# Performance work log

Hardware: AMD Instinct MI355X
Metric: run time of the kernel (lower is better)

The kernel has to match this reference:

```python
import jax, jax.numpy as jnp
import numpy as np

B, S, D = 2, 4096, 512   # batch, seq_len, hidden_dim
H, E = 8, 64             # n_heads, head_dim


def setup_inputs() -> dict:
    key = jax.random.key(0)
    ks = jax.random.split(key, 14)
    s = 0.02  # init scale
    return {
        "x":  jax.random.normal(ks[0], (B, S, D), dtype=jnp.float32),
        # stacked per-head projection weights, stored as [H, in, out]
        "wq": jax.random.normal(ks[1], (H, D, E), dtype=jnp.float32) * s,
        "bq": jax.random.normal(ks[2], (H, E), dtype=jnp.float32) * s,
        "wk": jax.random.normal(ks[3], (H, D, E), dtype=jnp.float32) * s,
        "bk": jax.random.normal(ks[4], (H, E), dtype=jnp.float32) * s,
        "wv": jax.random.normal(ks[5], (H, D, E), dtype=jnp.float32) * s,
        "bv": jax.random.normal(ks[6], (H, E), dtype=jnp.float32) * s,
        "wo": jax.random.normal(ks[7], (H, E, D), dtype=jnp.float32) * s,
        "bo": jax.random.normal(ks[8], (H, D), dtype=jnp.float32) * s,
        # MLP: Linear(D,D) -> ReLU -> Linear(D,D), stored as [in, out]
        "w1": jax.random.normal(ks[9], (D, D), dtype=jnp.float32) * s,
        "b1": jax.random.normal(ks[10], (D,), dtype=jnp.float32) * s,
        "w2": jax.random.normal(ks[11], (D, D), dtype=jnp.float32) * s,
        "b2": jax.random.normal(ks[12], (D,), dtype=jnp.float32) * s,
    }


def reference(x, wq, bq, wk, bk, wv, bv, wo, bo, w1, b1, w2, b2):
    # Per-head projections, batched over heads: [B, H, S, E]
    q = jnp.einsum('bsd,hde->bhse', x, wq) + bq[None, :, None, :]
    k = jnp.einsum('bsd,hde->bhse', x, wk) + bk[None, :, None, :]
    v = jnp.einsum('bsd,hde->bhse', x, wv) + bv[None, :, None, :]
    scale = 1.0 / jnp.sqrt(jnp.asarray(q.shape[-1], q.dtype))
    scores = jnp.einsum('bhse,bhte->bhst', q, k) * scale  # [B,H,S,S]
    A = jax.nn.softmax(scores, axis=-1)
    ctx = jnp.einsum('bhst,bhte->bhse', A, v)             # [B,H,S,E]
    # w_o per head then sum over heads (each head adds its bias once)
    y = jnp.einsum('bhse,hed->bsd', ctx, wo) + jnp.sum(bo, axis=0)
    # MLP
    h = jax.nn.relu(y @ w1 + b1)
    return h @ w2 + b2
```

## Files before the change

### kernel.cpp

```cpp
#include <hip/hip_runtime.h>
#include <math.h>

#define Bsz 2
#define Sq  4096
#define Dm  512
#define Hn  8
#define Eh  64

typedef unsigned short u16;
typedef __attribute__((ext_vector_type(8))) short bf16x8;
typedef __attribute__((ext_vector_type(4))) float f32x4;
typedef __attribute__((ext_vector_type(16))) float f32x16;
typedef __attribute__((ext_vector_type(4))) unsigned short u16x4;

#define KSCALE 0.18033688011112042f

__device__ __forceinline__ u16 f2bf(float f) {
    unsigned int u = __float_as_uint(f);
    u += 0x7FFFu + ((u >> 16) & 1u);
    return (u16)(u >> 16);
}

__device__ __forceinline__ float fast_exp2(float x) {
#if defined(__HIP_DEVICE_COMPILE__) && __has_builtin(__builtin_amdgcn_exp2f)
    return __builtin_amdgcn_exp2f(x);
#else
    return exp2f(x);
#endif
}

__device__ __forceinline__ f32x16 mfma_32x32x16(bf16x8 a, bf16x8 b, f32x16 c) {
#if defined(__HIP_DEVICE_COMPILE__)
    return __builtin_amdgcn_mfma_f32_32x32x16_bf16(a, b, c, 0, 0, 0);
#else
    (void)a; (void)b;
    return c;
#endif
}

__device__ __forceinline__ unsigned cvt_pk_bf16(float lo, float hi) {
#if defined(__HIP_DEVICE_COMPILE__)
    unsigned r;
    asm("v_cvt_pk_bf16_f32 %0, %1, %2" : "=v"(r) : "v"(lo), "v"(hi));
    return r;
#else
    return ((unsigned)f2bf(hi) << 16) | (unsigned)f2bf(lo);
#endif
}

__device__ __forceinline__ void plane32_swap(unsigned &a, unsigned &b) {
#if defined(__HIP_DEVICE_COMPILE__)
    asm volatile("v_permlane32_swap_b32 %0, %1" : "+v"(a), "+v"(b));
#endif
}

__device__ __forceinline__ bf16x8 frag_of(unsigned a, unsigned b, unsigned c, unsigned d) {
    union { unsigned u[4]; bf16x8 v; } r;
    r.u[0] = a; r.u[1] = b; r.u[2] = c; r.u[3] = d;
    return r.v;
}

__device__ __forceinline__ void async16(const u16* g, u16* l) {
    __builtin_amdgcn_global_load_lds(
        (const __attribute__((address_space(1))) void*)g,
        (__attribute__((address_space(3))) void*)l, 16, 0, 0);
}

template<int TN, int NT>
__device__ __forceinline__ void gemm_core(
    const u16* __restrict__ A, const u16* __restrict__ WT,
    int m0, int n0, u16* Ast, u16* Bst, f32x4 (&acc)[4][NT])
{
    const int tid  = threadIdx.x;
    const int lane = tid & 63, wid = tid >> 6;
    const int l15  = lane & 15, quad = lane >> 4;
    const int wm = wid >> 1, wn = wid & 1;

    for (int kt = 0; kt < Dm / 64; ++kt) {
        const int k0 = kt * 64;
        __syncthreads();
#pragma unroll
        for (int j = 0; j < 4; ++j) {
            int ci = wid * 256 + j * 64 + lane;
            int row = ci >> 3, c = (ci & 7) ^ (row & 7);
            async16(&A[(size_t)(m0 + row) * Dm + k0 + c * 8],
                    &Ast[(size_t)(wid * 256 + j * 64) * 8]);
        }
#pragma unroll
        for (int j = 0; j < TN / 32; ++j) {
            int ci = wid * (TN * 2) + j * 64 + lane;
            int row = ci >> 3, c = (ci & 7) ^ (row & 7);
            async16(&WT[(size_t)(n0 + row) * Dm + k0 + c * 8],
                    &Bst[(size_t)(wid * (TN * 2) + j * 64) * 8]);
        }
        __syncthreads();
#pragma unroll
        for (int ks = 0; ks < 2; ++ks) {
            bf16x8 af[4], bfr[NT];
#pragma unroll
            for (int mt = 0; mt < 4; ++mt) {
                int r = wm * 64 + mt * 16 + l15;
                af[mt] = *(const bf16x8*)&Ast[(r * 8 + ((ks * 4 + quad) ^ (r & 7))) * 8];
            }
#pragma unroll
            for (int nt = 0; nt < NT; ++nt) {
                int n = wn * (TN / 2) + nt * 16 + l15;
                bfr[nt] = *(const bf16x8*)&Bst[(n * 8 + ((ks * 4 + quad) ^ (n & 7))) * 8];
            }
#pragma unroll
            for (int mt = 0; mt < 4; ++mt)
#pragma unroll
                for (int nt = 0; nt < NT; ++nt)
                    acc[mt][nt] = __builtin_amdgcn_mfma_f32_16x16x32_bf16(
                        af[mt], bfr[nt], acc[mt][nt], 0, 0, 0);
        }
    }
}

__global__ __launch_bounds__(256) void prep_kernel(
    const float* __restrict__ x,
    const float* __restrict__ wq, const float* __restrict__ wk,
    const float* __restrict__ wv, const float* __restrict__ wo,
    const float* __restrict__ w1, const float* __restrict__ w2,
    const float* __restrict__ bo,
    u16* __restrict__ xb, u16* __restrict__ wqkvT, u16* __restrict__ woT,
    u16* __restrict__ w1T, u16* __restrict__ w2T, float* __restrict__ bo_s)
{
    const int seg = blockIdx.y, bx = blockIdx.x, tid = threadIdx.x;
    if (seg == 0) {
        const float4* xi = (const float4*)x;
        for (int i = bx * 256 + tid; i < (Bsz * Sq * Dm) / 4; i += 64 * 256) {
            float4 v = xi[i];
            u16x4 o = {f2bf(v.x), f2bf(v.y), f2bf(v.z), f2bf(v.w)};
            *(u16x4*)&xb[(size_t)i * 4] = o;
        }
        return;
    }
    if (seg == 7) {
        int d = bx * 256 + tid;
        if (d < Dm) {
            float s = 0.0f;
#pragma unroll
            for (int h = 0; h < Hn; ++h) s += bo[h * Dm + d];
            bo_s[d] = s;
        }
        return;
    }
    __shared__ float t[64][65];
    const float* src; u16* dst; int ld_in;
    if (seg <= 3) {
        const float* w = (seg == 1) ? wq : (seg == 2) ? wk : wv;
        int head = bx >> 3, kt = bx & 7;
        src = w + (size_t)head * Dm * Eh + (size_t)kt * 64 * 64;
        ld_in = 64;
        dst = wqkvT + ((size_t)((seg - 1) * 8 + head) * 64) * 512 + kt * 64;
    } else {
        const float* w = (seg == 4) ? wo : (seg == 5) ? w1 : w2;
        u16* dT = (seg == 4) ? woT : (seg == 5) ? w1T : w2T;
        int tr = bx >> 3, tc = bx & 7;
        src = w + (size_t)(tr * 64) * 512 + tc * 64;
        ld_in = 512;
        dst = dT + (size_t)(tc * 64) * 512 + tr * 64;
    }
#pragma unroll
    for (int it = 0; it < 16; ++it) {
        int idx = it * 256 + tid;
        int r = idx >> 6, c = idx & 63;
        t[r][c] = src[(size_t)r * ld_in + c];
    }
    __syncthreads();
#pragma unroll
    for (int it = 0; it < 4; ++it) {
        int idx = it * 256 + tid;
        int oc = idx >> 4, og = idx & 15;
        u16x4 o;
#pragma unroll
        for (int j = 0; j < 4; ++j) o[j] = f2bf(t[og * 4 + j][oc]);
        *(u16x4*)&dst[(size_t)oc * 512 + og * 4] = o;
    }
}

__global__ __launch_bounds__(256, 2) void qkv_gemm(
    const u16* __restrict__ xb, const u16* __restrict__ wqkvT,
    const float* __restrict__ bq, const float* __restrict__ bk,
    const float* __restrict__ bv,
    u16* __restrict__ qb, u16* __restrict__ kb, u16* __restrict__ vbT)
{
    __shared__ __align__(16) u16 Ast[128 * 64];
    __shared__ __align__(16) u16 Bst[64 * 64];
    const int proj = blockIdx.y >> 3, h = blockIdx.y & 7;
    const u16* WT = wqkvT + (size_t)blockIdx.y * 64 * 512;

    f32x4 acc[4][2];
#pragma unroll
    for (int i = 0; i < 4; ++i)
#pragma unroll
        for (int j = 0; j < 2; ++j) acc[i][j] = (f32x4)0.0f;

    gemm_core<64, 2>(xb, WT, blockIdx.x * 128, 0, Ast, Bst, acc);

    const int tid = threadIdx.x;
    const int lane = tid & 63, wid = tid >> 6;
    const int l15 = lane & 15, quad = lane >> 4;
    const int wm = wid >> 1, wn = wid & 1;
    const float* bias = (proj == 0) ? bq : (proj == 1) ? bk : bv;

    const int mbase = blockIdx.x * 128 + wm * 64;
    const int b = mbase >> 12;
    const int sbase = (mbase & (Sq - 1));
    const int bh = b * Hn + h;

#pragma unroll
    for (int mt = 0; mt < 4; ++mt)
#pragma unroll
        for (int nt = 0; nt < 2; ++nt) {
            int e = wn * 32 + nt * 16 + l15;
            float bval = bias[h * Eh + e];
            int s = sbase + mt * 16 + quad * 4;
            if (proj == 2) {
                u16x4 o;
#pragma unroll
                for (int r = 0; r < 4; ++r) o[r] = f2bf(acc[mt][nt][r] + bval);
                *(u16x4*)&vbT[((size_t)bh * Eh + e) * Sq + s] = o;
            } else if (proj == 1) {
                for (int r = 0; r < 4; ++r)
                    kb[((size_t)bh * Sq + s + r) * Eh + e] =
                        f2bf((acc[mt][nt][r] + bval) * KSCALE);
            } else {
                for (int r = 0; r < 4; ++r)
                    qb[((size_t)bh * Sq + s + r) * Eh + e] = f2bf(acc[mt][nt][r] + bval);
            }
        }
}

__global__ __launch_bounds__(256, 2) void attn_kernel(
    const u16* __restrict__ qb, const u16* __restrict__ kb,
    const u16* __restrict__ vbT, u16* __restrict__ ctxb)
{
    __shared__ __align__(16) u16 kst[2][128 * 64];
    __shared__ __align__(16) u16 vst[2][64 * 128];

    const int tid  = threadIdx.x;
    const int lane = tid & 63, wid = tid >> 6;
    const int l31  = lane & 31, hh = lane >> 5;
    const int bh = blockIdx.y;
    const int q0 = blockIdx.x * 128;
    const int b = bh >> 3, h = bh & 7;

    const u16* qg = qb + (size_t)bh * Sq * Eh;
    const u16* kg = kb + (size_t)bh * Sq * Eh;
    const u16* vg = vbT + (size_t)bh * Eh * Sq;

    int krow[4], kcol[4], vrow[4], vcol[4];
#pragma unroll
    for (int j = 0; j < 4; ++j) {
        int ci = wid * 256 + j * 64 + lane;
        krow[j] = ci >> 3;
        kcol[j] = (ci & 7) ^ (krow[j] & 7);
        vrow[j] = ci >> 4;
        int vc  = ci & 15;
        vcol[j] = (vc & 8) | ((vc & 7) ^ (vrow[j] & 7));
    }

    bf16x8 qf[4];
    {
        const u16* qrow = &qg[(size_t)(q0 + wid * 32 + l31) * Eh + hh * 8];
#pragma unroll
        for (int ks = 0; ks < 4; ++ks)
            qf[ks] = *(const bf16x8*)&qrow[ks * 16];
    }

    f32x16 O[2];
    O[0] = (f32x16)0.0f;
    O[1] = (f32x16)0.0f;
    float lp = 0.0f;

#pragma unroll
    for (int j = 0; j < 4; ++j) {
        async16(&kg[(size_t)krow[j] * Eh + kcol[j] * 8],
                &kst[0][(wid * 256 + j * 64) * 8]);
        async16(&vg[(size_t)vrow[j] * Sq + vcol[j] * 8],
                &vst[0][(wid * 256 + j * 64) * 8]);
    }

    const int t7 = l31 & 7;

    for (int kt = 0; kt < Sq / 128; ++kt) {
        const int cur = kt & 1;
        __syncthreads();

        if (kt < Sq / 128 - 1) {
            const int t1 = (kt + 1) * 128;
#pragma unroll
            for (int j = 0; j < 4; ++j) {
                async16(&kg[(size_t)(t1 + krow[j]) * Eh + kcol[j] * 8],
                        &kst[cur ^ 1][(wid * 256 + j * 64) * 8]);
                async16(&vg[(size_t)vrow[j] * Sq + t1 + vcol[j] * 8],
                        &vst[cur ^ 1][(wid * 256 + j * 64) * 8]);
            }
        }

        const u16* kcur = kst[cur];
        const u16* vcur = vst[cur];

#pragma unroll
        for (int tt = 0; tt < 4; ++tt) {
            f32x16 S = (f32x16)0.0f;
            const int trow = (tt * 32 + l31) * 64;
#pragma unroll
            for (int ks = 0; ks < 4; ++ks) {
                bf16x8 kf = *(const bf16x8*)&kcur[trow + ((ks * 2 + hh) ^ t7) * 8];
                S = mfma_32x32x16(kf, qf[ks], S);
            }

            unsigned px[8];
#pragma unroll
            for (int j = 0; j < 8; ++j) {
                float p0 = fast_exp2(S[2 * j]);
                float p1 = fast_exp2(S[2 * j + 1]);
                lp += p0 + p1;
                px[j] = cvt_pk_bf16(p0, p1);
            }
            plane32_swap(px[0], px[2]);
            plane32_swap(px[1], px[3]);
            plane32_swap(px[4], px[6]);
            plane32_swap(px[5], px[7]);
            bf16x8 f0 = frag_of(px[0], px[1], px[2], px[3]);
            bf16x8 f1 = frag_of(px[4], px[5], px[6], px[7]);

#pragma unroll
            for (int et = 0; et < 2; ++et) {
                const int erow = (et * 32 + l31) * 128;
                int c0 = tt * 4 + hh;
                int c1 = c0 + 2;
                int g0 = (c0 & 8) | ((c0 & 7) ^ t7);
                int g1 = (c1 & 8) | ((c1 & 7) ^ t7);
                bf16x8 v0 = *(const bf16x8*)&vcur[erow + g0 * 8];
                bf16x8 v1 = *(const bf16x8*)&vcur[erow + g1 * 8];
                O[et] = mfma_32x32x16(v0, f0, O[et]);
                O[et] = mfma_32x32x16(v1, f1, O[et]);
            }
        }
    }

    lp += __shfl_xor(lp, 32, 64);
    const float rl = 1.0f / lp;

    const int qglob = q0 + wid * 32 + l31;
    u16* crow = ctxb + ((size_t)(b * Sq + qglob) * Hn + h) * Eh;
#pragma unroll
    for (int et = 0; et < 2; ++et)
#pragma unroll
        for (int g = 0; g < 4; ++g) {
            u16x4 o;
#pragma unroll
            for (int i = 0; i < 4; ++i) o[i] = f2bf(O[et][g * 4 + i] * rl);
            *(u16x4*)&crow[et * 32 + g * 8 + hh * 4] = o;
        }
}

template<int MODE>
__global__ __launch_bounds__(256, 2) void gemmMN(
    const u16* __restrict__ A, const u16* __restrict__ WT,
    const float* __restrict__ bias, void* __restrict__ Cout)
{
    __shared__ __align__(16) u16 Ast[128 * 64];
    __shared__ __align__(16) u16 Bst[64 * 64];

    f32x4 acc[4][2];
#pragma unroll
    for (int i = 0; i < 4; ++i)
#pragma unroll
        for (int j = 0; j < 2; ++j) acc[i][j] = (f32x4)0.0f;

    gemm_core<64, 2>(A, WT, blockIdx.x * 128, blockIdx.y * 64, Ast, Bst, acc);

    const int tid = threadIdx.x;
    const int lane = tid & 63, wid = tid >> 6;
    const int l15 = lane & 15, quad = lane >> 4;
    const int m0 = blockIdx.x * 128 + (wid >> 1) * 64;
    const int n0 = blockIdx.y * 64 + (wid & 1) * 32;

#pragma unroll
    for (int mt = 0; mt < 4; ++mt)
#pragma unroll
        for (int nt = 0; nt < 2; ++nt) {
            int col = n0 + nt * 16 + l15;
            float bval = bias[col];
#pragma unroll
            for (int r = 0; r < 4; ++r) {
                int row = m0 + mt * 16 + quad * 4 + r;
                float v = acc[mt][nt][r] + bval;
                if (MODE == 1) v = fmaxf(v, 0.0f);
                if (MODE == 2) ((float*)Cout)[(size_t)row * Dm + col] = v;
                else           ((u16*)Cout)[(size_t)row * Dm + col] = f2bf(v);
            }
        }
}

extern "C" void kernel_launch(void* const* d_in, const int* in_sizes, int n_in,
                              void* d_out, int out_size, void* d_ws, size_t ws_size,
                              hipStream_t stream)
{
    const float* x  = (const float*)d_in[0];
    const float* wq = (const float*)d_in[1];
    const float* bq = (const float*)d_in[2];
    const float* wk = (const float*)d_in[3];
    const float* bk = (const float*)d_in[4];
    const float* wv = (const float*)d_in[5];
    const float* bv = (const float*)d_in[6];
    const float* wo = (const float*)d_in[7];
    const float* bo = (const float*)d_in[8];
    const float* w1 = (const float*)d_in[9];
    const float* b1 = (const float*)d_in[10];
    const float* w2 = (const float*)d_in[11];
    const float* b2 = (const float*)d_in[12];
    float* out = (float*)d_out;
    char* wsb = (char*)d_ws;

    const size_t MB = 1u << 20;
    u16*   xb    = (u16*)(wsb + 0);
    u16*   qb    = (u16*)(wsb + 8 * MB);
    u16*   kb    = (u16*)(wsb + 16 * MB);
    u16*   vbT   = (u16*)(wsb + 24 * MB);
    u16*   ctxb  = (u16*)(wsb + 32 * MB);
    u16*   ybuf  = (u16*)(wsb + 40 * MB);
    u16*   h1    = (u16*)(wsb + 48 * MB);
    u16*   wqkvT = (u16*)(wsb + 56 * MB);
    u16*   woT   = (u16*)(wsb + 58 * MB);
    u16*   w1T   = (u16*)(wsb + 59 * MB);
    u16*   w2T   = (u16*)(wsb + 60 * MB);
    float* bo_s  = (float*)(wsb + 61 * MB);

    prep_kernel<<<dim3(64, 8), 256, 0, stream>>>(
        x, wq, wk, wv, wo, w1, w2, bo, xb, wqkvT, woT, w1T, w2T, bo_s);
    qkv_gemm<<<dim3(Sq * Bsz / 128, 24), 256, 0, stream>>>(
        xb, wqkvT, bq, bk, bv, qb, kb, vbT);
    attn_kernel<<<dim3(Sq / 128, Bsz * Hn), 256, 0, stream>>>(qb, kb, vbT, ctxb);
    gemmMN<0><<<dim3(Bsz * Sq / 128, Dm / 64), 256, 0, stream>>>(ctxb, woT, bo_s, ybuf);
    gemmMN<1><<<dim3(Bsz * Sq / 128, Dm / 64), 256, 0, stream>>>(ybuf, w1T, b1, h1);
    gemmMN<2><<<dim3(Bsz * Sq / 128, Dm / 64), 256, 0, stream>>>(h1, w2T, b2, out);
}
```

Baseline: 239.4 us.

## Split attention key tiles across two wave groups and compute row sums via MFMA

The attention kernel grows from 256 to 512 threads. Two groups of four waves each process half of every 128-key tile for the same queries, and their partial outputs and row sums are combined through shared memory at the end. The per-lane scalar softmax-denominator accumulation is replaced by an MFMA against a ones vector, which moves that VALU work onto the matrix unit. This raises waves per block and per-CU parallelism, at the cost of an extra reduction with two barriers, two more MFMAs per tile, and the denominator now being summed from bf16-rounded probabilities.

New measurement: 236.1 us. Within noise of the previous version (-1.4%).

```diff
diff --git a/kernel.cpp b/kernel.cpp
--- a/kernel.cpp
+++ b/kernel.cpp
@@ -233,7 +233,7 @@
         }
 }
 
-__global__ __launch_bounds__(256, 2) void attn_kernel(
+__global__ __launch_bounds__(512, 4) void attn_kernel(
     const u16* __restrict__ qb, const u16* __restrict__ kb,
     const u16* __restrict__ vbT, u16* __restrict__ ctxb)
 {
@@ -242,6 +242,7 @@
 
     const int tid  = threadIdx.x;
     const int lane = tid & 63, wid = tid >> 6;
+    const int wq = wid & 3, wt = wid >> 2;
     const int l31  = lane & 31, hh = lane >> 5;
     const int bh = blockIdx.y;
     const int q0 = blockIdx.x * 128;
@@ -251,10 +252,10 @@
     const u16* kg = kb + (size_t)bh * Sq * Eh;
     const u16* vg = vbT + (size_t)bh * Eh * Sq;
 
-    int krow[4], kcol[4], vrow[4], vcol[4];
-#pragma unroll
-    for (int j = 0; j < 4; ++j) {
-        int ci = wid * 256 + j * 64 + lane;
+    int krow[2], kcol[2], vrow[2], vcol[2];
+#pragma unroll
+    for (int j = 0; j < 2; ++j) {
+        int ci = wid * 128 + j * 64 + lane;
         krow[j] = ci >> 3;
         kcol[j] = (ci & 7) ^ (krow[j] & 7);
         vrow[j] = ci >> 4;
@@ -264,23 +265,30 @@
 
     bf16x8 qf[4];
     {
-        const u16* qrow = &qg[(size_t)(q0 + wid * 32 + l31) * Eh + hh * 8];
+        const u16* qrow = &qg[(size_t)(q0 + wq * 32 + l31) * Eh + hh * 8];
 #pragma unroll
         for (int ks = 0; ks < 4; ++ks)
             qf[ks] = *(const bf16x8*)&qrow[ks * 16];
     }
 
-    f32x16 O[2];
+    bf16x8 ones;
+    {
+        union { unsigned u[4]; bf16x8 v; } t;
+        t.u[0] = t.u[1] = t.u[2] = t.u[3] = 0x3F803F80u;
+        ones = t.v;
+    }
+
+    f32x16 O[2], lsum;
     O[0] = (f32x16)0.0f;
     O[1] = (f32x16)0.0f;
-    float lp = 0.0f;
-
-#pragma unroll
-    for (int j = 0; j < 4; ++j) {
+    lsum = (f32x16)0.0f;
+
+#pragma unroll
+    for (int j = 0; j < 2; ++j) {
         async16(&kg[(size_t)krow[j] * Eh + kcol[j] * 8],
-                &kst[0][(wid * 256 + j * 64) * 8]);
+                &kst[0][(wid * 128 + j * 64) * 8]);
         async16(&vg[(size_t)vrow[j] * Sq + vcol[j] * 8],
-                &vst[0][(wid * 256 + j * 64) * 8]);
+                &vst[0][(wid * 128 + j * 64) * 8]);
     }
 
     const int t7 = l31 & 7;
@@ -292,11 +300,11 @@
         if (kt < Sq / 128 - 1) {
             const int t1 = (kt + 1) * 128;
 #pragma unroll
-            for (int j = 0; j < 4; ++j) {
+            for (int j = 0; j < 2; ++j) {
                 async16(&kg[(size_t)(t1 + krow[j]) * Eh + kcol[j] * 8],
-                        &kst[cur ^ 1][(wid * 256 + j * 64) * 8]);
+                        &kst[cur ^ 1][(wid * 128 + j * 64) * 8]);
                 async16(&vg[(size_t)vrow[j] * Sq + t1 + vcol[j] * 8],
-                        &vst[cur ^ 1][(wid * 256 + j * 64) * 8]);
+                        &vst[cur ^ 1][(wid * 128 + j * 64) * 8]);
             }
         }
 
@@ -304,7 +312,8 @@
         const u16* vcur = vst[cur];
 
 #pragma unroll
-        for (int tt = 0; tt < 4; ++tt) {
+        for (int tts = 0; tts < 2; ++tts) {
+            const int tt = wt * 2 + tts;
             f32x16 S = (f32x16)0.0f;
             const int trow = (tt * 32 + l31) * 64;
 #pragma unroll
@@ -318,7 +327,6 @@
             for (int j = 0; j < 8; ++j) {
                 float p0 = fast_exp2(S[2 * j]);
                 float p1 = fast_exp2(S[2 * j + 1]);
-                lp += p0 + p1;
                 px[j] = cvt_pk_bf16(p0, p1);
             }
             plane32_swap(px[0], px[2]);
@@ -327,6 +335,9 @@
             plane32_swap(px[5], px[7]);
             bf16x8 f0 = frag_of(px[0], px[1], px[2], px[3]);
             bf16x8 f1 = frag_of(px[4], px[5], px[6], px[7]);
+
+            lsum = mfma_32x32x16(ones, f0, lsum);
+            lsum = mfma_32x32x16(ones, f1, lsum);
 
 #pragma unroll
             for (int et = 0; et < 2; ++et) {
@@ -343,20 +354,47 @@
         }
     }
 
-    lp += __shfl_xor(lp, 32, 64);
-    const float rl = 1.0f / lp;
-
-    const int qglob = q0 + wid * 32 + l31;
-    u16* crow = ctxb + ((size_t)(b * Sq + qglob) * Hn + h) * Eh;
-#pragma unroll
-    for (int et = 0; et < 2; ++et)
-#pragma unroll
-        for (int g = 0; g < 4; ++g) {
-            u16x4 o;
-#pragma unroll
-            for (int i = 0; i < 4; ++i) o[i] = f2bf(O[et][g * 4 + i] * rl);
-            *(u16x4*)&crow[et * 32 + g * 8 + hh * 4] = o;
-        }
+    __syncthreads();
+    float* redO = (float*)&kst[0][0];
+    float* redL = (float*)&vst[0][0];
+    const int rbase = (wq * 64 + lane) * 32;
+    if (wt == 1) {
+#pragma unroll
+        for (int et = 0; et < 2; ++et)
+#pragma unroll
+            for (int c = 0; c < 4; ++c) {
+                f32x4 v4;
+#pragma unroll
+                for (int i = 0; i < 4; ++i) v4[i] = O[et][c * 4 + i];
+                *(f32x4*)&redO[rbase + (((et * 4 + c) ^ (lane & 7)) * 4)] = v4;
+            }
+        redL[wq * 64 + lane] = lsum[0];
+    }
+    __syncthreads();
+    if (wt == 0) {
+#pragma unroll
+        for (int et = 0; et < 2; ++et)
+#pragma unroll
+            for (int c = 0; c < 4; ++c) {
+                f32x4 v4 = *(const f32x4*)&redO[rbase + (((et * 4 + c) ^ (lane & 7)) * 4)];
+#pragma unroll
+                for (int i = 0; i < 4; ++i) O[et][c * 4 + i] += v4[i];
+            }
+        const float lp = lsum[0] + redL[wq * 64 + lane];
+        const float rl = 1.0f / lp;
+
+        const int qglob = q0 + wq * 32 + l31;
+        u16* crow = ctxb + ((size_t)(b * Sq + qglob) * Hn + h) * Eh;
+#pragma unroll
+        for (int et = 0; et < 2; ++et)
+#pragma unroll
+            for (int g = 0; g < 4; ++g) {
+                u16x4 o;
+#pragma unroll
+                for (int i = 0; i < 4; ++i) o[i] = f2bf(O[et][g * 4 + i] * rl);
+                *(u16x4*)&crow[et * 32 + g * 8 + hh * 4] = o;
+            }
+    }
 }
 
 template<int MODE>
@@ -436,7 +474,7 @@
         x, wq, wk, wv, wo, w1, w2, bo, xb, wqkvT, woT, w1T, w2T, bo_s);
     qkv_gemm<<<dim3(Sq * Bsz / 128, 24), 256, 0, stream>>>(
         xb, wqkvT, bq, bk, bv, qb, kb, vbT);
-    attn_kernel<<<dim3(Sq / 128, Bsz * Hn), 256, 0, stream>>>(qb, kb, vbT, ctxb);
+    attn_kernel<<<dim3(Sq / 128, Bsz * Hn), 512, 0, stream>>>(qb, kb, vbT, ctxb);
     gemmMN<0><<<dim3(Bsz * Sq / 128, Dm / 64), 256, 0, stream>>>(ctxb, woT, bo_s, ybuf);
     gemmMN<1><<<dim3(Bsz * Sq / 128, Dm / 64), 256, 0, stream>>>(ybuf, w1T, b1, h1);
     gemmMN<2><<<dim3(Bsz * Sq / 128, Dm / 64), 256, 0, stream>>>(h1, w2T, b2, out);
```
